# Kernel tuning notes

Hardware: AMD Instinct MI355X
Metric: run time of the kernel (lower is better)

## Reference

```python
import jax, jax.numpy as jnp
import numpy as np

LN_EPS = 1e-5

def setup_inputs() -> dict:
    key = jax.random.key(0)
    ks = jax.random.split(key, 7)
    B, S, D = 16, 2048, 512
    scale_g = 1.0 / np.sqrt(2 * D)
    scale_c = 1.0 / np.sqrt(2 * D)
    return {
        "points": jax.random.normal(ks[0], (B, S, D), dtype=jnp.float32),
        "W_gate": jax.random.uniform(ks[1], (2 * D, 2 * D), jnp.float32, -scale_g, scale_g),
        "b_gate": jax.random.uniform(ks[2], (2 * D,), jnp.float32, -scale_g, scale_g),
        "W_cand": jax.random.uniform(ks[3], (2 * D, D), jnp.float32, -scale_c, scale_c),
        "b_cand": jax.random.uniform(ks[4], (D,), jnp.float32, -scale_c, scale_c),
        "gamma": jnp.ones((D,), jnp.float32),
        "beta": jnp.zeros((D,), jnp.float32),
    }

def _layer_norm(x, gamma, beta):
    mu = jnp.mean(x, axis=-1, keepdims=True)
    var = jnp.mean(jnp.square(x - mu), axis=-1, keepdims=True)
    return (x - mu) * jax.lax.rsqrt(var + LN_EPS) * gamma + beta

def reference(points, W_gate, b_gate, W_cand, b_cand, gamma, beta):
    B, S, D = points.shape
    h0 = jnp.zeros((B, D), dtype=points.dtype)

    def step(h, p_t):  # p_t: [B, D]
        combined = jnp.concatenate([p_t, h], axis=1)          # [B, 2D]
        gates = combined @ W_gate + b_gate                    # [B, 2D]
        r = jax.nn.sigmoid(gates[:, :D])
        z = jax.nn.sigmoid(gates[:, D:])
        cand_in = jnp.concatenate([p_t, r * h], axis=1)       # [B, 2D]
        c = jnp.tanh(cand_in @ W_cand + b_cand)               # [B, D]
        h_new = (1.0 - z) * h + z * c
        return h_new, h_new

    _, states = jax.lax.scan(step, h0, jnp.swapaxes(points, 0, 1))  # [S, B, D]
    states = jnp.swapaxes(states, 0, 1)                             # [B, S, D]
    displacement = states - points
    deformed = points + displacement
    return _layer_norm(deformed, gamma, beta)
```

## Files before the change

kernel.cpp:

```cpp
#include <hip/hip_runtime.h>


typedef _Float16 half8 __attribute__((ext_vector_type(8)));
typedef _Float16 half4 __attribute__((ext_vector_type(4)));
typedef float floatx4 __attribute__((ext_vector_type(4)));
typedef int int4v __attribute__((ext_vector_type(4)));

#define NBLK 16
#define TPB 256
#define S_LEN 2048

#define SZ_WPK (96ull * 16 * 64 * 8 * 2)
#define OFF_WHPK 0ull
#define OFF_WXPK (OFF_WHPK + SZ_WPK)
#define OFF_HBUF (OFF_WXPK + SZ_WPK)
#define OFF_CNT (OFF_HBUF + 16384ull)
#define OFF_RH (OFF_CNT + 16384ull)
#define OFF_XGT (OFF_RH + 16384ull)

__device__ __forceinline__ float sigmoid_f(float x) {
  return 1.f / (1.f + __expf(-x));
}
__device__ __forceinline__ float tanh_f(float x) {
  x = fminf(15.f, fmaxf(-15.f, x));
  float e = __expf(2.f * x);
  return (e - 1.f) / (e + 1.f);
}

__device__ __forceinline__ void ldfrag_cg(const _Float16* p, int4v (&f)[16]) {
  asm volatile(
      "global_load_dwordx4 %0,  %16, off sc0 sc1\n\t"
      "global_load_dwordx4 %1,  %16, off offset:64 sc0 sc1\n\t"
      "global_load_dwordx4 %2,  %16, off offset:128 sc0 sc1\n\t"
      "global_load_dwordx4 %3,  %16, off offset:192 sc0 sc1\n\t"
      "global_load_dwordx4 %4,  %16, off offset:256 sc0 sc1\n\t"
      "global_load_dwordx4 %5,  %16, off offset:320 sc0 sc1\n\t"
      "global_load_dwordx4 %6,  %16, off offset:384 sc0 sc1\n\t"
      "global_load_dwordx4 %7,  %16, off offset:448 sc0 sc1\n\t"
      "global_load_dwordx4 %8,  %16, off offset:512 sc0 sc1\n\t"
      "global_load_dwordx4 %9,  %16, off offset:576 sc0 sc1\n\t"
      "global_load_dwordx4 %10, %16, off offset:640 sc0 sc1\n\t"
      "global_load_dwordx4 %11, %16, off offset:704 sc0 sc1\n\t"
      "global_load_dwordx4 %12, %16, off offset:768 sc0 sc1\n\t"
      "global_load_dwordx4 %13, %16, off offset:832 sc0 sc1\n\t"
      "global_load_dwordx4 %14, %16, off offset:896 sc0 sc1\n\t"
      "global_load_dwordx4 %15, %16, off offset:960 sc0 sc1\n\t"
      "s_waitcnt vmcnt(0)"
      : "=&v"(f[0]), "=&v"(f[1]), "=&v"(f[2]), "=&v"(f[3]), "=&v"(f[4]),
        "=&v"(f[5]), "=&v"(f[6]), "=&v"(f[7]), "=&v"(f[8]), "=&v"(f[9]),
        "=&v"(f[10]), "=&v"(f[11]), "=&v"(f[12]), "=&v"(f[13]), "=&v"(f[14]),
        "=&v"(f[15])
      : "v"(p)
      : "memory");
}
__device__ __forceinline__ void st_cg_u16(_Float16* p, _Float16 v) {
  unsigned u = (unsigned)__builtin_bit_cast(unsigned short, v);
  asm volatile("global_store_short %0, %1, off sc0 sc1" ::"v"(p), "v"(u)
               : "memory");
}
__device__ __forceinline__ void vwait() {
  asm volatile("s_waitcnt vmcnt(0)" ::: "memory");
}

__device__ __forceinline__ void gbar(unsigned* __restrict__ cnt, int idx) {
  __syncthreads();
  if (threadIdx.x == 0) {
    __hip_atomic_fetch_add(&cnt[idx], 1u, __ATOMIC_RELAXED,
                           __HIP_MEMORY_SCOPE_AGENT);
    while (__hip_atomic_load(&cnt[idx], __ATOMIC_RELAXED,
                             __HIP_MEMORY_SCOPE_AGENT) < (unsigned)NBLK) {
    }
  }
  __syncthreads();
}

__global__ void pack_kernel(const float* __restrict__ Wg,
                            const float* __restrict__ Wc,
                            _Float16* __restrict__ Whpk,
                            _Float16* __restrict__ Wxpk) {
  int unit = blockIdx.x * 4 + (threadIdx.x >> 6);
  int lane = threadIdx.x & 63;
  int set = (unit >= 1536) ? 1 : 0;
  int rem = unit - set * 1536;
  int tile = rem >> 4, kc = rem & 15;
  int kb = kc * 32 + ((lane >> 4) << 3);
  int n = lane & 15;
  int row0 = set ? 0 : 512;
  half8 w;
  if (tile < 64) {
    int col = tile * 16 + n;
#pragma unroll
    for (int jj = 0; jj < 8; ++jj)
      w[jj] = (_Float16)Wg[(size_t)(row0 + kb + jj) * 1024 + col];
  } else {
    int col = (tile - 64) * 16 + n;
#pragma unroll
    for (int jj = 0; jj < 8; ++jj)
      w[jj] = (_Float16)Wc[(size_t)(row0 + kb + jj) * 512 + col];
  }
  _Float16* dst = set ? Wxpk : Whpk;
  *(half8*)(dst + ((size_t)rem * 64 + lane) * 8) = w;
}

__global__ __launch_bounds__(TPB) void xgemm_kernel(
    const float* __restrict__ points, const float* __restrict__ b_gate,
    const float* __restrict__ b_cand, const _Float16* __restrict__ Wxpk,
    _Float16* __restrict__ xgt) {
  __shared__ _Float16 x_lds[16][520];
  const int tid = threadIdx.x;
  const int wave = tid >> 6, lane = tid & 63;
  const int ln15 = lane & 15, q = lane >> 4;
  const int t = blockIdx.x;
  const int m = tid & 15, ch = tid >> 4;

  const float* xp = points + ((size_t)m * S_LEN + t) * 512 + ch * 32;
#pragma unroll
  for (int u = 0; u < 4; ++u) {
    float4 f0 = ((const float4*)xp)[2 * u];
    float4 f1 = ((const float4*)xp)[2 * u + 1];
    half8 hv;
    hv[0] = (_Float16)f0.x; hv[1] = (_Float16)f0.y;
    hv[2] = (_Float16)f0.z; hv[3] = (_Float16)f0.w;
    hv[4] = (_Float16)f1.x; hv[5] = (_Float16)f1.y;
    hv[6] = (_Float16)f1.z; hv[7] = (_Float16)f1.w;
    *(half8*)&x_lds[m][ch * 32 + u * 8] = hv;
  }
  __syncthreads();

  for (int tile = wave; tile < 96; tile += 4) {
    const _Float16* W = Wxpk + (size_t)tile * 8192;
    floatx4 a0 = {0.f, 0.f, 0.f, 0.f}, a1 = {0.f, 0.f, 0.f, 0.f};
#pragma unroll
    for (int kc = 0; kc < 16; kc += 2) {
      a0 = __builtin_amdgcn_mfma_f32_16x16x32_f16(
          *(const half8*)&x_lds[ln15][kc * 32 + q * 8],
          *(const half8*)(W + ((size_t)kc * 64 + lane) * 8), a0, 0, 0, 0);
      a1 = __builtin_amdgcn_mfma_f32_16x16x32_f16(
          *(const half8*)&x_lds[ln15][(kc + 1) * 32 + q * 8],
          *(const half8*)(W + ((size_t)(kc + 1) * 64 + lane) * 8), a1, 0, 0, 0);
    }
    float bias = (tile < 64) ? b_gate[tile * 16 + ln15]
                             : b_cand[(tile - 64) * 16 + ln15];
    half4 o;
#pragma unroll
    for (int i = 0; i < 4; ++i) o[i] = (_Float16)(a0[i] + a1[i] + bias);
    *(half4*)(xgt + (((size_t)t * 96 + tile) * 16 + ln15) * 16 + q * 4) = o;
  }
}

__global__ __launch_bounds__(TPB, 1) void rec_kernel(
    const _Float16* __restrict__ Whpk, const _Float16* __restrict__ xgt,
    _Float16* __restrict__ h_buf, _Float16* __restrict__ rh_buf,
    unsigned* __restrict__ cnt, float* __restrict__ out) {
  __shared__ float z_lds[16][36];

  const int tid = threadIdx.x;
  const int wave = tid >> 6, lane = tid & 63;
  const int ln15 = lane & 15, q = lane >> 4;
  const int j = blockIdx.x;

  const int twA = (wave < 2) ? (2 * j + wave) : (32 + 2 * j + (wave - 2));
  const int twB = 64 + 2 * j + (wave & 1);
  const int colA = 32 * j + 16 * (wave & 1) + ln15;

  half8 wA[16], wB[16];
  {
    const _Float16* sA = Whpk + (size_t)twA * 8192 + lane * 8;
#pragma unroll
    for (int kc = 0; kc < 16; ++kc) wA[kc] = *(const half8*)(sA + kc * 512);
  }
  if (wave < 2) {
    const _Float16* sB = Whpk + (size_t)twB * 8192 + lane * 8;
#pragma unroll
    for (int kc = 0; kc < 16; ++kc) wB[kc] = *(const half8*)(sB + kc * 512);
  }

  const _Float16* hA_base = h_buf + ln15 * 512 + q * 8;
  const _Float16* rhA_base = rh_buf + ln15 * 512 + q * 8;
  _Float16* rh_st = rh_buf + (q * 4) * 512 + colA;
  _Float16* h_st = h_buf + (q * 4) * 512 + colA;

  float hreg[4] = {0.f, 0.f, 0.f, 0.f};

  for (int t = 0; t < S_LEN; ++t) {
    half4 xga =
        *(const half4*)(xgt + (((size_t)t * 96 + twA) * 16 + ln15) * 16 + q * 4);

    int4v hf[16];
    ldfrag_cg(hA_base, hf);
    floatx4 a0 = {0.f, 0.f, 0.f, 0.f}, a1 = {0.f, 0.f, 0.f, 0.f};
#pragma unroll
    for (int kc = 0; kc < 16; kc += 2) {
      a0 = __builtin_amdgcn_mfma_f32_16x16x32_f16(
          __builtin_bit_cast(half8, hf[kc]), wA[kc], a0, 0, 0, 0);
      a1 = __builtin_amdgcn_mfma_f32_16x16x32_f16(
          __builtin_bit_cast(half8, hf[kc + 1]), wA[kc + 1], a1, 0, 0, 0);
    }
    if (wave < 2) {
#pragma unroll
      for (int i = 0; i < 4; ++i) {
        float r = sigmoid_f(a0[i] + a1[i] + (float)xga[i]);
        st_cg_u16(rh_st + i * 512, (_Float16)(r * hreg[i]));
      }
      vwait();
    } else {
#pragma unroll
      for (int i = 0; i < 4; ++i)
        z_lds[q * 4 + i][16 * (wave - 2) + ln15] =
            sigmoid_f(a0[i] + a1[i] + (float)xga[i]);
    }
    gbar(cnt, 2 * t);

    if (wave < 2) {
      half4 xcb = *(const half4*)(xgt + (((size_t)t * 96 + twB) * 16 + ln15) * 16 +
                                  q * 4);
      int4v rf[16];
      ldfrag_cg(rhA_base, rf);
      floatx4 b0 = {0.f, 0.f, 0.f, 0.f}, b1 = {0.f, 0.f, 0.f, 0.f};
#pragma unroll
      for (int kc = 0; kc < 16; kc += 2) {
        b0 = __builtin_amdgcn_mfma_f32_16x16x32_f16(
            __builtin_bit_cast(half8, rf[kc]), wB[kc], b0, 0, 0, 0);
        b1 = __builtin_amdgcn_mfma_f32_16x16x32_f16(
            __builtin_bit_cast(half8, rf[kc + 1]), wB[kc + 1], b1, 0, 0, 0);
      }
#pragma unroll
      for (int i = 0; i < 4; ++i) {
        float cv = tanh_f(b0[i] + b1[i] + (float)xcb[i]);
        float zz = z_lds[q * 4 + i][16 * wave + ln15];
        float hn = hreg[i] + zz * (cv - hreg[i]);
        _Float16 hh = (_Float16)hn;
        hreg[i] = (float)hh;
        st_cg_u16(h_st + i * 512, hh);
        out[((size_t)(q * 4 + i) * S_LEN + t) * 512 + colA] = hn;
      }
      vwait();
    }
    gbar(cnt, 2 * t + 1);
  }
}

__global__ void ln_kernel(float* __restrict__ out, const float* __restrict__ gamma,
                          const float* __restrict__ beta) {
  int gw = (blockIdx.x * blockDim.x + threadIdx.x) >> 6;
  int lane = threadIdx.x & 63;
  int nw = (gridDim.x * blockDim.x) >> 6;
  float4 ga = ((const float4*)(gamma + lane * 8))[0];
  float4 gb = ((const float4*)(gamma + lane * 8))[1];
  float4 ba = ((const float4*)(beta + lane * 8))[0];
  float4 bb = ((const float4*)(beta + lane * 8))[1];
  for (int r = gw; r < 16 * S_LEN; r += nw) {
    float* p = out + (size_t)r * 512 + lane * 8;
    float4 v0 = ((float4*)p)[0], v1 = ((float4*)p)[1];
    float s = v0.x + v0.y + v0.z + v0.w + v1.x + v1.y + v1.z + v1.w;
    float sq = v0.x * v0.x + v0.y * v0.y + v0.z * v0.z + v0.w * v0.w +
               v1.x * v1.x + v1.y * v1.y + v1.z * v1.z + v1.w * v1.w;
#pragma unroll
    for (int off = 32; off > 0; off >>= 1) {
      s += __shfl_xor(s, off);
      sq += __shfl_xor(sq, off);
    }
    float mean = s * (1.f / 512.f);
    float var = sq * (1.f / 512.f) - mean * mean;
    float rstd = rsqrtf(var + 1e-5f);
    v0.x = (v0.x - mean) * rstd * ga.x + ba.x;
    v0.y = (v0.y - mean) * rstd * ga.y + ba.y;
    v0.z = (v0.z - mean) * rstd * ga.z + ba.z;
    v0.w = (v0.w - mean) * rstd * ga.w + ba.w;
    v1.x = (v1.x - mean) * rstd * gb.x + bb.x;
    v1.y = (v1.y - mean) * rstd * gb.y + bb.y;
    v1.z = (v1.z - mean) * rstd * gb.z + bb.z;
    v1.w = (v1.w - mean) * rstd * gb.w + bb.w;
    ((float4*)p)[0] = v0;
    ((float4*)p)[1] = v1;
  }
}

extern "C" void kernel_launch(void* const* d_in, const int* in_sizes, int n_in,
                              void* d_out, int out_size, void* d_ws,
                              size_t ws_size, hipStream_t stream) {
  const float* points = (const float*)d_in[0];
  const float* W_gate = (const float*)d_in[1];
  const float* b_gate = (const float*)d_in[2];
  const float* W_cand = (const float*)d_in[3];
  const float* b_cand = (const float*)d_in[4];
  const float* gamma = (const float*)d_in[5];
  const float* beta = (const float*)d_in[6];
  char* ws = (char*)d_ws;
  _Float16* Whpk = (_Float16*)(ws + OFF_WHPK);
  _Float16* Wxpk = (_Float16*)(ws + OFF_WXPK);
  _Float16* h_buf = (_Float16*)(ws + OFF_HBUF);
  unsigned* cnt = (unsigned*)(ws + OFF_CNT);
  _Float16* rh_buf = (_Float16*)(ws + OFF_RH);
  _Float16* xgt = (_Float16*)(ws + OFF_XGT);
  float* out = (float*)d_out;

  hipMemsetAsync(ws + OFF_HBUF, 0, 32768, stream);
  pack_kernel<<<768, 256, 0, stream>>>(W_gate, W_cand, Whpk, Wxpk);
  xgemm_kernel<<<S_LEN, TPB, 0, stream>>>(points, b_gate, b_cand, Wxpk, xgt);
  rec_kernel<<<NBLK, TPB, 0, stream>>>(Whpk, xgt, h_buf, rh_buf, cnt, out);
  ln_kernel<<<512, 256, 0, stream>>>(out, gamma, beta);
}
```

Measured before the change: 13.45 ms.

## Replace counter grid barrier with per-block flags and stage h via LDS

```diff
diff --git a/kernel.cpp b/kernel.cpp
--- a/kernel.cpp
+++ b/kernel.cpp
@@ -27,29 +27,14 @@
   return (e - 1.f) / (e + 1.f);
 }
 
-__device__ __forceinline__ void ldfrag_cg(const _Float16* p, int4v (&f)[16]) {
+__device__ __forceinline__ void ld4_cg(const _Float16* p, int4v (&f)[4]) {
   asm volatile(
-      "global_load_dwordx4 %0,  %16, off sc0 sc1\n\t"
-      "global_load_dwordx4 %1,  %16, off offset:64 sc0 sc1\n\t"
-      "global_load_dwordx4 %2,  %16, off offset:128 sc0 sc1\n\t"
-      "global_load_dwordx4 %3,  %16, off offset:192 sc0 sc1\n\t"
-      "global_load_dwordx4 %4,  %16, off offset:256 sc0 sc1\n\t"
-      "global_load_dwordx4 %5,  %16, off offset:320 sc0 sc1\n\t"
-      "global_load_dwordx4 %6,  %16, off offset:384 sc0 sc1\n\t"
-      "global_load_dwordx4 %7,  %16, off offset:448 sc0 sc1\n\t"
-      "global_load_dwordx4 %8,  %16, off offset:512 sc0 sc1\n\t"
-      "global_load_dwordx4 %9,  %16, off offset:576 sc0 sc1\n\t"
-      "global_load_dwordx4 %10, %16, off offset:640 sc0 sc1\n\t"
-      "global_load_dwordx4 %11, %16, off offset:704 sc0 sc1\n\t"
-      "global_load_dwordx4 %12, %16, off offset:768 sc0 sc1\n\t"
-      "global_load_dwordx4 %13, %16, off offset:832 sc0 sc1\n\t"
-      "global_load_dwordx4 %14, %16, off offset:896 sc0 sc1\n\t"
-      "global_load_dwordx4 %15, %16, off offset:960 sc0 sc1\n\t"
+      "global_load_dwordx4 %0, %4, off sc0 sc1\n\t"
+      "global_load_dwordx4 %1, %4, off offset:64 sc0 sc1\n\t"
+      "global_load_dwordx4 %2, %4, off offset:128 sc0 sc1\n\t"
+      "global_load_dwordx4 %3, %4, off offset:192 sc0 sc1\n\t"
       "s_waitcnt vmcnt(0)"
-      : "=&v"(f[0]), "=&v"(f[1]), "=&v"(f[2]), "=&v"(f[3]), "=&v"(f[4]),
-        "=&v"(f[5]), "=&v"(f[6]), "=&v"(f[7]), "=&v"(f[8]), "=&v"(f[9]),
-        "=&v"(f[10]), "=&v"(f[11]), "=&v"(f[12]), "=&v"(f[13]), "=&v"(f[14]),
-        "=&v"(f[15])
+      : "=&v"(f[0]), "=&v"(f[1]), "=&v"(f[2]), "=&v"(f[3])
       : "v"(p)
       : "memory");
 }
@@ -61,14 +46,29 @@
 __device__ __forceinline__ void vwait() {
   asm volatile("s_waitcnt vmcnt(0)" ::: "memory");
 }
-
-__device__ __forceinline__ void gbar(unsigned* __restrict__ cnt, int idx) {
+__device__ __forceinline__ void st_flag(unsigned* p, unsigned v) {
+  asm volatile("global_store_dword %0, %1, off sc0 sc1" ::"v"(p), "v"(v)
+               : "memory");
+}
+__device__ __forceinline__ unsigned ld_flag(const unsigned* p) {
+  unsigned v;
+  asm volatile("global_load_dword %0, %1, off sc0 sc1\n\t"
+               "s_waitcnt vmcnt(0)"
+               : "=v"(v)
+               : "v"(p)
+               : "memory");
+  return v;
+}
+
+__device__ __forceinline__ void gbar(unsigned* __restrict__ flags, int j,
+                                     unsigned token, int wave, int lane) {
   __syncthreads();
-  if (threadIdx.x == 0) {
-    __hip_atomic_fetch_add(&cnt[idx], 1u, __ATOMIC_RELAXED,
-                           __HIP_MEMORY_SCOPE_AGENT);
-    while (__hip_atomic_load(&cnt[idx], __ATOMIC_RELAXED,
-                             __HIP_MEMORY_SCOPE_AGENT) < (unsigned)NBLK) {
+  if (wave == 0) {
+    if (lane == 0) st_flag(flags + j, token);
+    const unsigned* fp = flags + (lane & 15);
+    for (;;) {
+      unsigned v = ld_flag(fp);
+      if (__all((int)(v >= token))) break;
     }
   }
   __syncthreads();
@@ -151,7 +151,8 @@
 __global__ __launch_bounds__(TPB, 1) void rec_kernel(
     const _Float16* __restrict__ Whpk, const _Float16* __restrict__ xgt,
     _Float16* __restrict__ h_buf, _Float16* __restrict__ rh_buf,
-    unsigned* __restrict__ cnt, float* __restrict__ out) {
+    unsigned* __restrict__ flags, float* __restrict__ out) {
+  __shared__ int4v hsh[1024];
   __shared__ float z_lds[16][36];
 
   const int tid = threadIdx.x;
@@ -175,26 +176,38 @@
     for (int kc = 0; kc < 16; ++kc) wB[kc] = *(const half8*)(sB + kc * 512);
   }
 
-  const _Float16* hA_base = h_buf + ln15 * 512 + q * 8;
-  const _Float16* rhA_base = rh_buf + ln15 * 512 + q * 8;
+  const _Float16* h_stage = h_buf + ln15 * 512 + q * 8 + wave * 128;
+  const _Float16* rh_stage = rh_buf + ln15 * 512 + q * 8 + wave * 128;
   _Float16* rh_st = rh_buf + (q * 4) * 512 + colA;
   _Float16* h_st = h_buf + (q * 4) * 512 + colA;
 
+  const _Float16* xga_p = xgt + ((size_t)twA * 16 + ln15) * 16 + q * 4;
+  const _Float16* xcb_p = xgt + ((size_t)twB * 16 + ln15) * 16 + q * 4;
+  half4 xga = *(const half4*)xga_p;
+  half4 xcb = {0, 0, 0, 0};
+  if (wave < 2) xcb = *(const half4*)xcb_p;
+
   float hreg[4] = {0.f, 0.f, 0.f, 0.f};
 
   for (int t = 0; t < S_LEN; ++t) {
-    half4 xga =
-        *(const half4*)(xgt + (((size_t)t * 96 + twA) * 16 + ln15) * 16 + q * 4);
-
-    int4v hf[16];
-    ldfrag_cg(hA_base, hf);
+    const size_t pn = (size_t)((t + 1 < S_LEN) ? t + 1 : t) * 24576;
+
+    {
+      int4v f[4];
+      ld4_cg(h_stage, f);
+#pragma unroll
+      for (int u = 0; u < 4; ++u) hsh[(4 * wave + u) * 64 + lane] = f[u];
+    }
+    __syncthreads();
+
     floatx4 a0 = {0.f, 0.f, 0.f, 0.f}, a1 = {0.f, 0.f, 0.f, 0.f};
 #pragma unroll
     for (int kc = 0; kc < 16; kc += 2) {
       a0 = __builtin_amdgcn_mfma_f32_16x16x32_f16(
-          __builtin_bit_cast(half8, hf[kc]), wA[kc], a0, 0, 0, 0);
+          __builtin_bit_cast(half8, hsh[kc * 64 + lane]), wA[kc], a0, 0, 0, 0);
       a1 = __builtin_amdgcn_mfma_f32_16x16x32_f16(
-          __builtin_bit_cast(half8, hf[kc + 1]), wA[kc + 1], a1, 0, 0, 0);
+          __builtin_bit_cast(half8, hsh[(kc + 1) * 64 + lane]), wA[kc + 1], a1,
+          0, 0, 0);
     }
     if (wave < 2) {
 #pragma unroll
@@ -209,21 +222,28 @@
         z_lds[q * 4 + i][16 * (wave - 2) + ln15] =
             sigmoid_f(a0[i] + a1[i] + (float)xga[i]);
     }
-    gbar(cnt, 2 * t);
+    gbar(flags, j, 2u * t + 1u, wave, lane);
+
+    {
+      int4v f[4];
+      ld4_cg(rh_stage, f);
+#pragma unroll
+      for (int u = 0; u < 4; ++u) hsh[(4 * wave + u) * 64 + lane] = f[u];
+    }
+    __syncthreads();
 
     if (wave < 2) {
-      half4 xcb = *(const half4*)(xgt + (((size_t)t * 96 + twB) * 16 + ln15) * 16 +
-                                  q * 4);
-      int4v rf[16];
-      ldfrag_cg(rhA_base, rf);
       floatx4 b0 = {0.f, 0.f, 0.f, 0.f}, b1 = {0.f, 0.f, 0.f, 0.f};
 #pragma unroll
       for (int kc = 0; kc < 16; kc += 2) {
         b0 = __builtin_amdgcn_mfma_f32_16x16x32_f16(
-            __builtin_bit_cast(half8, rf[kc]), wB[kc], b0, 0, 0, 0);
+            __builtin_bit_cast(half8, hsh[kc * 64 + lane]), wB[kc], b0, 0, 0,
+            0);
         b1 = __builtin_amdgcn_mfma_f32_16x16x32_f16(
-            __builtin_bit_cast(half8, rf[kc + 1]), wB[kc + 1], b1, 0, 0, 0);
+            __builtin_bit_cast(half8, hsh[(kc + 1) * 64 + lane]), wB[kc + 1],
+            b1, 0, 0, 0);
       }
+      float hn_s[4];
 #pragma unroll
       for (int i = 0; i < 4; ++i) {
         float cv = tanh_f(b0[i] + b1[i] + (float)xcb[i]);
@@ -232,11 +252,18 @@
         _Float16 hh = (_Float16)hn;
         hreg[i] = (float)hh;
         st_cg_u16(h_st + i * 512, hh);
-        out[((size_t)(q * 4 + i) * S_LEN + t) * 512 + colA] = hn;
+        hn_s[i] = hn;
       }
       vwait();
-    }
-    gbar(cnt, 2 * t + 1);
+      xga = *(const half4*)(xga_p + pn);
+      xcb = *(const half4*)(xcb_p + pn);
+#pragma unroll
+      for (int i = 0; i < 4; ++i)
+        out[((size_t)(q * 4 + i) * S_LEN + t) * 512 + colA] = hn_s[i];
+    } else {
+      xga = *(const half4*)(xga_p + pn);
+    }
+    gbar(flags, j, 2u * t + 2u, wave, lane);
   }
 }
 
@@ -290,7 +317,7 @@
   _Float16* Whpk = (_Float16*)(ws + OFF_WHPK);
   _Float16* Wxpk = (_Float16*)(ws + OFF_WXPK);
   _Float16* h_buf = (_Float16*)(ws + OFF_HBUF);
-  unsigned* cnt = (unsigned*)(ws + OFF_CNT);
+  unsigned* flags = (unsigned*)(ws + OFF_CNT);
   _Float16* rh_buf = (_Float16*)(ws + OFF_RH);
   _Float16* xgt = (_Float16*)(ws + OFF_XGT);
   float* out = (float*)d_out;
@@ -298,6 +325,6 @@
   hipMemsetAsync(ws + OFF_HBUF, 0, 32768, stream);
   pack_kernel<<<768, 256, 0, stream>>>(W_gate, W_cand, Whpk, Wxpk);
   xgemm_kernel<<<S_LEN, TPB, 0, stream>>>(points, b_gate, b_cand, Wxpk, xgt);
-  rec_kernel<<<NBLK, TPB, 0, stream>>>(Whpk, xgt, h_buf, rh_buf, cnt, out);
+  rec_kernel<<<NBLK, TPB, 0, stream>>>(Whpk, xgt, h_buf, rh_buf, flags, out);
   ln_kernel<<<512, 256, 0, stream>>>(out, gamma, beta);
 }
```

Result: faster. 11.04 ms (-17.9%).
